# Optimization experiments

Hardware: AMD Instinct MI355X
Metric: run time of the kernel (lower is better)

## Reference

```python
import jax, jax.numpy as jnp
import numpy as np

N = 50000      # nodes
E = 800000     # edges (avg degree 16)
IN, HID, OUT = 256, 128, 64


def _glorot(key, shape):
    fan_in, fan_out = shape[0], shape[1]
    limit = np.sqrt(6.0 / (fan_in + fan_out))
    return jax.random.uniform(key, shape, jnp.float32, -limit, limit)


def setup_inputs() -> dict:
    key = jax.random.key(0)
    ks = jax.random.split(key, 8)
    x = jax.random.normal(ks[0], (N, IN), jnp.float32)
    edge_index = jax.random.randint(ks[1], (2, E), 0, N, dtype=jnp.int64)
    W1 = _glorot(ks[2], (IN, HID))
    b1 = jnp.zeros((HID,), jnp.float32)
    W2 = _glorot(ks[3], (HID, OUT))
    b2 = jnp.zeros((OUT,), jnp.float32)
    aw1 = _glorot(ks[4], (HID, 1))
    ab1 = jnp.zeros((1,), jnp.float32)
    aw2 = _glorot(ks[5], (OUT, 1))
    ab2 = jnp.zeros((1,), jnp.float32)
    return {"x": x, "edge_index": edge_index, "W1": W1, "b1": b1,
            "W2": W2, "b2": b2, "aw1": aw1, "ab1": ab1, "aw2": aw2, "ab2": ab2}


def gcn_conv(x, W, b, src, dst, n):
    # PyG GCNConv: add self-loops, symmetric degree normalization, then aggregate.
    h = x @ W                                   # [n, out]
    loops = jnp.arange(n, dtype=src.dtype)
    s = jnp.concatenate([src, loops])           # [E+n]
    d = jnp.concatenate([dst, loops])
    deg = jax.ops.segment_sum(jnp.ones(s.shape[0], h.dtype), d, num_segments=n)
    dinv = jnp.where(deg > 0, jax.lax.rsqrt(deg), 0.0)
    norm = dinv[s] * dinv[d]                    # [E+n]
    out = jax.ops.segment_sum(h[s] * norm[:, None], d, num_segments=n)
    return out + b


def reference(x, edge_index, W1, b1, W2, b2, aw1, ab1, aw2, ab2):
    # eval mode: dropout is identity
    src, dst = edge_index[0], edge_index[1]
    h = gcn_conv(x, W1, b1, src, dst, N)
    h = jax.nn.relu(h)
    h = h * jax.nn.sigmoid(h @ aw1 + ab1)       # sigmoid attention gate 1
    h = gcn_conv(h, W2, b2, src, dst, N)
    return h * jax.nn.sigmoid(h @ aw2 + ab2)    # sigmoid attention gate 2
```

## Files before the change

### kernel.cpp

```cpp
#include <hip/hip_runtime.h>
#include <math.h>

#define N_NODES 50000
#define N_EDGES 800000
#define D_IN    256
#define D_HID   128
#define D_OUT   64

#define NB 196
#define CH 4096

typedef unsigned int u32;
typedef unsigned short u16;
typedef __attribute__((ext_vector_type(8))) short bf16x8;
typedef __attribute__((ext_vector_type(4))) float f32x4;

__device__ __forceinline__ float bflo(u32 u) {
    union { u32 i; float f; } c; c.i = u << 16; return c.f;
}
__device__ __forceinline__ float bfhi(u32 u) {
    union { u32 i; float f; } c; c.i = u & 0xffff0000u; return c.f;
}
__device__ __forceinline__ u32 pack_bf2(float a, float b) {
    union { float f; u32 i; } ca, cb; ca.f = a; cb.f = b;
    u32 ra = (ca.i + 0x7fffu + ((ca.i >> 16) & 1u)) >> 16;
    u32 rb = (cb.i + 0x7fffu + ((cb.i >> 16) & 1u)) & 0xffff0000u;
    return ra | rb;
}
__device__ __forceinline__ u32 bf16_rne(float f) {
    union { float f; u32 i; } c; c.f = f;
    return (c.i + 0x7fffu + ((c.i >> 16) & 1u)) >> 16;
}
__device__ __forceinline__ float bfbits_to_f32(u32 hb) {
    union { u32 i; float f; } c; c.i = hb << 16; return c.f;
}

__device__ __forceinline__ int edge_at(const void* ei, int is64, int which, int i) {
    if (is64) return (int)((const long long*)ei)[(size_t)which * N_EDGES + i];
    return ((const int*)ei)[which * N_EDGES + i];
}

__device__ __forceinline__ int detect_is64(const void* ei, int t, int* s_is32) {
    if (t == 0) *s_is32 = 0;
    __syncthreads();
    if (t < 256) {
        int vv = ((const int*)ei)[2 * t + 1];
        if (vv != 0) atomicOr(s_is32, 1);
    }
    __syncthreads();
    return (*s_is32 == 0);
}


__global__ __launch_bounds__(256) void k_hist(const void* __restrict__ ei,
                                              int* __restrict__ bcnt) {
    __shared__ int h[NB];
    __shared__ int s_is32;
    int t = threadIdx.x;
    int is64 = detect_is64(ei, t, &s_is32);
    for (int i = t; i < NB; i += 256) h[i] = 0;
    __syncthreads();
    for (int i = blockIdx.x * 256 + t; i < N_EDGES; i += gridDim.x * 256) {
        int d = edge_at(ei, is64, 1, i);
        atomicAdd(&h[d >> 8], 1);
    }
    __syncthreads();
    for (int i = t; i < NB; i += 256) if (h[i]) atomicAdd(&bcnt[i], h[i]);
}

__global__ void k_bscan(const int* __restrict__ bcnt, int* __restrict__ bstart,
                        int* __restrict__ bcur) {
    __shared__ int sm[256];
    int t = threadIdx.x;
    int v = (t < NB) ? bcnt[t] : 0;
    sm[t] = v; __syncthreads();
    for (int off = 1; off < 256; off <<= 1) {
        int a = (t >= off) ? sm[t - off] : 0;
        __syncthreads();
        sm[t] += a;
        __syncthreads();
    }
    if (t < NB) { bstart[t] = sm[t] - v; bcur[t] = sm[t] - v; }
}

__global__ __launch_bounds__(256) void k_scatter1(const void* __restrict__ ei,
                                                  int* __restrict__ bcur,
                                                  u32* __restrict__ ebuf) {
    __shared__ int h[NB], gbase[NB], lc[NB];
    __shared__ int s_is32;
    int t = threadIdx.x;
    int is64 = detect_is64(ei, t, &s_is32);
    for (int i = t; i < NB; i += 256) { h[i] = 0; lc[i] = 0; }
    __syncthreads();
    int base = blockIdx.x * CH;

    u32 p[CH / 256];
    #pragma unroll
    for (int j = 0; j < CH / 256; ++j) {
        int i = base + j * 256 + t;
        if (i < N_EDGES) {
            int s = edge_at(ei, is64, 0, i);
            int d = edge_at(ei, is64, 1, i);
            p[j] = (u32)s | ((u32)d << 16);
            atomicAdd(&h[d >> 8], 1);
        }
    }
    __syncthreads();
    for (int i = t; i < NB; i += 256) if (h[i]) gbase[i] = atomicAdd(&bcur[i], h[i]);
    __syncthreads();
    #pragma unroll
    for (int j = 0; j < CH / 256; ++j) {
        int i = base + j * 256 + t;
        if (i < N_EDGES) {
            int b = (int)(p[j] >> 24);
            int lp = atomicAdd(&lc[b], 1);
            ebuf[gbase[b] + lp] = p[j];
        }
    }
}

__global__ __launch_bounds__(256) void k_scatter2(const u32* __restrict__ ebuf,
                                                  const int* __restrict__ bstart,
                                                  const int* __restrict__ bcnt,
                                                  int* __restrict__ rowstart,
                                                  int* __restrict__ cnt,
                                                  float* __restrict__ dinv,
                                                  int* __restrict__ colidx) {
    __shared__ int h2[256], lofs[256], cur[256], sm[256];
    int b = blockIdx.x, t = threadIdx.x;
    int e0 = bstart[b], ne = bcnt[b];
    h2[t] = 0; cur[t] = 0;
    __syncthreads();
    for (int i = t; i < ne; i += 256) {
        u32 p = ebuf[e0 + i];
        atomicAdd(&h2[(p >> 16) & 255], 1);
    }
    __syncthreads();
    int v = h2[t]; sm[t] = v; __syncthreads();
    for (int off = 1; off < 256; off <<= 1) {
        int a = (t >= off) ? sm[t - off] : 0;
        __syncthreads();
        sm[t] += a;
        __syncthreads();
    }
    lofs[t] = sm[t] - v;
    __syncthreads();
    int node = (b << 8) + t;
    if (node < N_NODES) {
        rowstart[node] = e0 + lofs[t];
        cnt[node] = v;
        dinv[node] = rsqrtf(1.0f + (float)v);
    }
    for (int i = t; i < ne; i += 256) {
        u32 p = ebuf[e0 + i];
        int dl = (p >> 16) & 255;
        int lp = atomicAdd(&cur[dl], 1);
        colidx[e0 + lofs[dl] + lp] = (int)(p & 0xffffu);
    }
}

__global__ void k_wsplit(const float* __restrict__ W1, u16* __restrict__ t1h,
                         u16* __restrict__ t1l, const float* __restrict__ W2,
                         u16* __restrict__ t2h, u16* __restrict__ t2l) {
    int i = blockIdx.x * 256 + threadIdx.x;
    if (i < D_IN * D_HID) {
        int k = i / D_HID, c = i - k * D_HID;
        float f = W1[i];
        u32 hb = bf16_rne(f);
        u32 lb = bf16_rne(f - bfbits_to_f32(hb));
        t1h[(size_t)c * D_IN + k] = (u16)hb;
        t1l[(size_t)c * D_IN + k] = (u16)lb;
    }
    int j = i - D_IN * D_HID;
    if (j >= 0 && j < D_HID * D_OUT) {
        int k = j / D_OUT, c = j - k * D_OUT;
        float f = W2[j];
        u32 hb = bf16_rne(f);
        u32 lb = bf16_rne(f - bfbits_to_f32(hb));
        t2h[(size_t)c * D_HID + k] = (u16)hb;
        t2l[(size_t)c * D_HID + k] = (u16)lb;
    }
}

template <int K, int NF>
__global__ __launch_bounds__(256) void k_gemm_mfma(
    const float* __restrict__ A, const u16* __restrict__ tHi,
    const u16* __restrict__ tLo, const float* __restrict__ dinv,
    u32* __restrict__ Cp, int M) {
    constexpr int NT = NF / 16;
    constexpr int LDK = 40;
    __shared__ u16 aH[128][LDK], aL[128][LDK];
    __shared__ u16 wH[NF][LDK], wL[NF][LDK];

    const int t = threadIdx.x;
    const int lane = t & 63, wv = t >> 6;
    const int m0 = blockIdx.x * 128;
    const int lr = lane & 15, lk = (lane >> 4) * 8;

    f32x4 acc[2][NT] = {};

    const int arow = t >> 1;
    const int akq = (t & 1) * 16;
    const bool aok = (m0 + arow) < M;
    const float* asrc = A + (size_t)(m0 + arow) * K + akq;

    for (int ks = 0; ks < K; ks += 32) {
        {
            float buf[16];
            #pragma unroll
            for (int j = 0; j < 16; ++j) buf[j] = 0.0f;
            if (aok) {
                const float4* p = (const float4*)(asrc + ks);
                float4 v0 = p[0], v1 = p[1], v2 = p[2], v3 = p[3];
                buf[0] = v0.x; buf[1] = v0.y; buf[2]  = v0.z; buf[3]  = v0.w;
                buf[4] = v1.x; buf[5] = v1.y; buf[6]  = v1.z; buf[7]  = v1.w;
                buf[8] = v2.x; buf[9] = v2.y; buf[10] = v2.z; buf[11] = v2.w;
                buf[12] = v3.x; buf[13] = v3.y; buf[14] = v3.z; buf[15] = v3.w;
            }
            u32 h[16], l[16];
            #pragma unroll
            for (int j = 0; j < 16; ++j) {
                h[j] = bf16_rne(buf[j]);
                l[j] = bf16_rne(buf[j] - bfbits_to_f32(h[j]));
            }
            uint4 hv0 = make_uint4(h[0] | (h[1] << 16), h[2] | (h[3] << 16),
                                   h[4] | (h[5] << 16), h[6] | (h[7] << 16));
            uint4 hv1 = make_uint4(h[8] | (h[9] << 16), h[10] | (h[11] << 16),
                                   h[12] | (h[13] << 16), h[14] | (h[15] << 16));
            uint4 lv0 = make_uint4(l[0] | (l[1] << 16), l[2] | (l[3] << 16),
                                   l[4] | (l[5] << 16), l[6] | (l[7] << 16));
            uint4 lv1 = make_uint4(l[8] | (l[9] << 16), l[10] | (l[11] << 16),
                                   l[12] | (l[13] << 16), l[14] | (l[15] << 16));
            *(uint4*)&aH[arow][akq + 0] = hv0;
            *(uint4*)&aH[arow][akq + 8] = hv1;
            *(uint4*)&aL[arow][akq + 0] = lv0;
            *(uint4*)&aL[arow][akq + 8] = lv1;
        }
        #pragma unroll
        for (int idx = t; idx < NF * 4; idx += 256) {
            int col = idx >> 2;
            int k8 = (idx & 3) * 8;
            *(uint4*)&wH[col][k8] = *(const uint4*)&tHi[(size_t)col * K + ks + k8];
            *(uint4*)&wL[col][k8] = *(const uint4*)&tLo[(size_t)col * K + ks + k8];
        }
        __syncthreads();

        bf16x8 afH[2], afL[2];
        #pragma unroll
        for (int mt = 0; mt < 2; ++mt) {
            int r = wv * 32 + mt * 16 + lr;
            afH[mt] = *(const bf16x8*)&aH[r][lk];
            afL[mt] = *(const bf16x8*)&aL[r][lk];
        }
        #pragma unroll
        for (int nt = 0; nt < NT; ++nt) {
            bf16x8 bh = *(const bf16x8*)&wH[nt * 16 + lr][lk];
            bf16x8 bl = *(const bf16x8*)&wL[nt * 16 + lr][lk];
            #pragma unroll
            for (int mt = 0; mt < 2; ++mt) {
                acc[mt][nt] = __builtin_amdgcn_mfma_f32_16x16x32_bf16(afH[mt], bh, acc[mt][nt], 0, 0, 0);
                acc[mt][nt] = __builtin_amdgcn_mfma_f32_16x16x32_bf16(afL[mt], bh, acc[mt][nt], 0, 0, 0);
                acc[mt][nt] = __builtin_amdgcn_mfma_f32_16x16x32_bf16(afH[mt], bl, acc[mt][nt], 0, 0, 0);
            }
        }
        __syncthreads();
    }

    #pragma unroll
    for (int mt = 0; mt < 2; ++mt) {
        #pragma unroll
        for (int r = 0; r < 4; ++r) {
            int row = m0 + wv * 32 + mt * 16 + (lane >> 4) * 4 + r;
            float dv = (row < M) ? dinv[row] : 0.0f;
            #pragma unroll
            for (int nt = 0; nt < NT; ++nt) {
                float v = acc[mt][nt][r] * dv;
                float vn = __shfl_xor(v, 1);
                if (!(lane & 1) && row < M) {
                    Cp[(size_t)row * (NF / 2) + nt * 8 + (lr >> 1)] = pack_bf2(v, vn);
                }
            }
        }
    }
}


__global__ __launch_bounds__(256) void k_agg1(
        const u32* __restrict__ hs, const int* __restrict__ rowstart,
        const int* __restrict__ cnt, const int* __restrict__ colidx,
        const float* __restrict__ dinv,
        const float* __restrict__ b, const float* __restrict__ aw,
        const float* __restrict__ ab, float* __restrict__ out) {
    int v = blockIdx.x * 4 + (threadIdx.x >> 6);
    int l = threadIdx.x & 63;
    if (v >= N_NODES) return;
    float dv = dinv[v];
    u32 su = hs[(size_t)v * 64 + l];
    float ax = bflo(su), ay = bfhi(su);
    int start = rowstart[v], len = cnt[v];
    const int* cx = colidx + start;
    int j = 0;
    for (; j + 8 <= len; j += 8) {
        int s0 = cx[j], s1 = cx[j + 1], s2 = cx[j + 2], s3 = cx[j + 3];
        int s4 = cx[j + 4], s5 = cx[j + 5], s6 = cx[j + 6], s7 = cx[j + 7];
        u32 u0 = hs[(size_t)s0 * 64 + l];
        u32 u1 = hs[(size_t)s1 * 64 + l];
        u32 u2 = hs[(size_t)s2 * 64 + l];
        u32 u3 = hs[(size_t)s3 * 64 + l];
        u32 u4 = hs[(size_t)s4 * 64 + l];
        u32 u5 = hs[(size_t)s5 * 64 + l];
        u32 u6 = hs[(size_t)s6 * 64 + l];
        u32 u7 = hs[(size_t)s7 * 64 + l];
        ax += bflo(u0) + bflo(u1) + bflo(u2) + bflo(u3)
            + bflo(u4) + bflo(u5) + bflo(u6) + bflo(u7);
        ay += bfhi(u0) + bfhi(u1) + bfhi(u2) + bfhi(u3)
            + bfhi(u4) + bfhi(u5) + bfhi(u6) + bfhi(u7);
    }
    for (; j + 4 <= len; j += 4) {
        int s0 = cx[j], s1 = cx[j + 1], s2 = cx[j + 2], s3 = cx[j + 3];
        u32 u0 = hs[(size_t)s0 * 64 + l];
        u32 u1 = hs[(size_t)s1 * 64 + l];
        u32 u2 = hs[(size_t)s2 * 64 + l];
        u32 u3 = hs[(size_t)s3 * 64 + l];
        ax += bflo(u0) + bflo(u1) + bflo(u2) + bflo(u3);
        ay += bfhi(u0) + bfhi(u1) + bfhi(u2) + bfhi(u3);
    }
    for (; j < len; ++j) {
        u32 u = hs[(size_t)cx[j] * 64 + l];
        ax += bflo(u); ay += bfhi(u);
    }
    float2 bp = ((const float2*)b)[l];
    ax = fmaxf(ax * dv + bp.x, 0.0f);
    ay = fmaxf(ay * dv + bp.y, 0.0f);
    float2 ap = ((const float2*)aw)[l];
    float p = ax * ap.x + ay * ap.y;
    for (int off = 32; off; off >>= 1) p += __shfl_xor(p, off);
    float g = 1.0f / (1.0f + expf(-(p + ab[0])));
    ((float2*)out)[(size_t)v * 64 + l] = make_float2(ax * g, ay * g);
}

__global__ __launch_bounds__(256) void k_agg2(
        const u32* __restrict__ hs, const int* __restrict__ rowstart,
        const int* __restrict__ cnt, const int* __restrict__ colidx,
        const float* __restrict__ dinv,
        const float* __restrict__ b, const float* __restrict__ aw,
        const float* __restrict__ ab, float* __restrict__ out) {
    int v = blockIdx.x * 4 + (threadIdx.x >> 6);
    int l = threadIdx.x & 63;
    if (v >= N_NODES) return;
    int c = l & 31, half = l >> 5;
    float dv = dinv[v];
    float ax = 0.0f, ay = 0.0f;
    if (half == 0) {
        u32 su = hs[(size_t)v * 32 + c];
        ax = bflo(su); ay = bfhi(su);
    }
    int start = rowstart[v], len = cnt[v];
    const int* cx = colidx + start;
    int j = half;
    for (; j + 6 < len; j += 8) {
        int s0 = cx[j], s1 = cx[j + 2], s2 = cx[j + 4], s3 = cx[j + 6];
        u32 u0 = hs[(size_t)s0 * 32 + c];
        u32 u1 = hs[(size_t)s1 * 32 + c];
        u32 u2 = hs[(size_t)s2 * 32 + c];
        u32 u3 = hs[(size_t)s3 * 32 + c];
        ax += bflo(u0) + bflo(u1) + bflo(u2) + bflo(u3);
        ay += bfhi(u0) + bfhi(u1) + bfhi(u2) + bfhi(u3);
    }
    for (; j + 2 < len; j += 4) {
        int s0 = cx[j], s1 = cx[j + 2];
        u32 u0 = hs[(size_t)s0 * 32 + c];
        u32 u1 = hs[(size_t)s1 * 32 + c];
        ax += bflo(u0) + bflo(u1);
        ay += bfhi(u0) + bfhi(u1);
    }
    if (j < len) {
        u32 u = hs[(size_t)cx[j] * 32 + c];
        ax += bflo(u); ay += bfhi(u);
    }
    ax += __shfl_xor(ax, 32);
    ay += __shfl_xor(ay, 32);
    float2 bp = ((const float2*)b)[c];
    ax = ax * dv + bp.x;
    ay = ay * dv + bp.y;
    float2 ap = ((const float2*)aw)[c];
    float p = ax * ap.x + ay * ap.y;
    for (int off = 16; off; off >>= 1) p += __shfl_xor(p, off);
    float g = 1.0f / (1.0f + expf(-(p + ab[0])));
    if (half == 0) ((float2*)out)[(size_t)v * 32 + c] = make_float2(ax * g, ay * g);
}


static inline size_t align_up(size_t x, size_t a) { return (x + a - 1) & ~(a - 1); }

extern "C" void kernel_launch(void* const* d_in, const int* in_sizes, int n_in,
                              void* d_out, int out_size, void* d_ws, size_t ws_size,
                              hipStream_t stream) {
    const float* x   = (const float*)d_in[0];
    const void*  ei  = d_in[1];
    const float* W1  = (const float*)d_in[2];
    const float* b1  = (const float*)d_in[3];
    const float* W2  = (const float*)d_in[4];
    const float* b2  = (const float*)d_in[5];
    const float* aw1 = (const float*)d_in[6];
    const float* ab1 = (const float*)d_in[7];
    const float* aw2 = (const float*)d_in[8];
    const float* ab2 = (const float*)d_in[9];
    float* out = (float*)d_out;

    char* w = (char*)d_ws;
    size_t off = 0;
    int*   bcnt     = (int*)(w + off); off = align_up(off + NB * 4, 256);
    int*   bstart   = (int*)(w + off); off = align_up(off + NB * 4, 256);
    int*   bcur     = (int*)(w + off); off = align_up(off + NB * 4, 256);
    int*   cnt      = (int*)(w + off); off = align_up(off + N_NODES * 4, 256);
    int*   rowstart = (int*)(w + off); off = align_up(off + N_NODES * 4, 256);
    float* dinv     = (float*)(w + off); off = align_up(off + N_NODES * 4, 256);
    u32*   ebuf     = (u32*)(w + off); off = align_up(off + (size_t)N_EDGES * 4, 256);
    int*   colidx   = (int*)(w + off); off = align_up(off + (size_t)N_EDGES * 4, 256);
    u32*   h1s      = (u32*)(w + off); off = align_up(off + (size_t)N_NODES * 64 * 4, 256);
    float* h1g      = (float*)(w + off); off = align_up(off + (size_t)N_NODES * D_HID * 4, 256);
    u32*   h2s      = (u32*)(w + off); off = align_up(off + (size_t)N_NODES * 32 * 4, 256);
    u16*   wt1h     = (u16*)(w + off); off = align_up(off + (size_t)D_IN * D_HID * 2, 256);
    u16*   wt1l     = (u16*)(w + off); off = align_up(off + (size_t)D_IN * D_HID * 2, 256);
    u16*   wt2h     = (u16*)(w + off); off = align_up(off + (size_t)D_HID * D_OUT * 2, 256);
    u16*   wt2l     = (u16*)(w + off); off = align_up(off + (size_t)D_HID * D_OUT * 2, 256);
    (void)ws_size; (void)out_size; (void)n_in; (void)in_sizes;

    hipMemsetAsync(bcnt, 0, NB * 4, stream);

    k_wsplit<<<(D_IN * D_HID + D_HID * D_OUT + 255) / 256, 256, 0, stream>>>(
        W1, wt1h, wt1l, W2, wt2h, wt2l);

    k_hist<<<256, 256, 0, stream>>>(ei, bcnt);
    k_bscan<<<1, 256, 0, stream>>>(bcnt, bstart, bcur);
    k_scatter1<<<(N_EDGES + CH - 1) / CH, 256, 0, stream>>>(ei, bcur, ebuf);
    k_scatter2<<<NB, 256, 0, stream>>>(ebuf, bstart, bcnt, rowstart, cnt, dinv, colidx);

    k_gemm_mfma<D_IN, D_HID><<<(N_NODES + 127) / 128, 256, 0, stream>>>(x, wt1h, wt1l, dinv, h1s, N_NODES);
    k_agg1<<<(N_NODES + 3) / 4, 256, 0, stream>>>(h1s, rowstart, cnt, colidx, dinv, b1, aw1, ab1, h1g);

    k_gemm_mfma<D_HID, D_OUT><<<(N_NODES + 127) / 128, 256, 0, stream>>>(h1g, wt2h, wt2l, dinv, h2s, N_NODES);
    k_agg2<<<(N_NODES + 3) / 4, 256, 0, stream>>>(h2s, rowstart, cnt, colidx, dinv, b2, aw2, ab2, out);
}
```

Before: 238.0 us.

## Fuse bucket scan into histogram, drop memset, shrink GEMM tile, truncate bf16 split

The bucket prefix scan moves into the last block of the histogram kernel, chosen with an atomic ticket counter, and the memset of the bucket counts moves into the weight-split kernel, removing two launches. The GEMM row tile shrinks from 128 to 64 rows per block, doubling the grid and halving per-thread accumulators. The bf16 hi/lo split switches from round-to-nearest to truncation, which is cheaper; since the lo term captures the residual, accuracy should stay close. It relies on correct threadfence/ticket ordering for the fused scan.

```diff
diff --git a/kernel.cpp b/kernel.cpp
--- a/kernel.cpp
+++ b/kernel.cpp
@@ -27,13 +27,6 @@
     u32 rb = (cb.i + 0x7fffu + ((cb.i >> 16) & 1u)) & 0xffff0000u;
     return ra | rb;
 }
-__device__ __forceinline__ u32 bf16_rne(float f) {
-    union { float f; u32 i; } c; c.f = f;
-    return (c.i + 0x7fffu + ((c.i >> 16) & 1u)) >> 16;
-}
-__device__ __forceinline__ float bfbits_to_f32(u32 hb) {
-    union { u32 i; float f; } c; c.i = hb << 16; return c.f;
-}
 
 __device__ __forceinline__ int edge_at(const void* ei, int is64, int which, int i) {
     if (is64) return (int)((const long long*)ei)[(size_t)which * N_EDGES + i];
@@ -53,9 +46,13 @@
 
 
 __global__ __launch_bounds__(256) void k_hist(const void* __restrict__ ei,
-                                              int* __restrict__ bcnt) {
+                                              int* __restrict__ bcnt,
+                                              int* __restrict__ bstart,
+                                              int* __restrict__ bcur,
+                                              int* __restrict__ tick) {
     __shared__ int h[NB];
     __shared__ int s_is32;
+    __shared__ int s_last;
     int t = threadIdx.x;
     int is64 = detect_is64(ei, t, &s_is32);
     for (int i = t; i < NB; i += 256) h[i] = 0;
@@ -66,21 +63,21 @@
     }
     __syncthreads();
     for (int i = t; i < NB; i += 256) if (h[i]) atomicAdd(&bcnt[i], h[i]);
-}
-
-__global__ void k_bscan(const int* __restrict__ bcnt, int* __restrict__ bstart,
-                        int* __restrict__ bcur) {
-    __shared__ int sm[256];
-    int t = threadIdx.x;
-    int v = (t < NB) ? bcnt[t] : 0;
-    sm[t] = v; __syncthreads();
-    for (int off = 1; off < 256; off <<= 1) {
-        int a = (t >= off) ? sm[t - off] : 0;
-        __syncthreads();
-        sm[t] += a;
-        __syncthreads();
-    }
-    if (t < NB) { bstart[t] = sm[t] - v; bcur[t] = sm[t] - v; }
+    __threadfence();
+    if (t == 0) s_last = (atomicAdd(tick, 1) == (int)gridDim.x - 1);
+    __syncthreads();
+    if (s_last) {
+        __shared__ int sm[256];
+        int v = (t < NB) ? atomicAdd(&bcnt[t], 0) : 0;
+        sm[t] = v; __syncthreads();
+        for (int off = 1; off < 256; off <<= 1) {
+            int a = (t >= off) ? sm[t - off] : 0;
+            __syncthreads();
+            sm[t] += a;
+            __syncthreads();
+        }
+        if (t < NB) { bstart[t] = sm[t] - v; bcur[t] = sm[t] - v; }
+    }
 }
 
 __global__ __launch_bounds__(256) void k_scatter1(const void* __restrict__ ei,
@@ -161,24 +158,27 @@
 
 __global__ void k_wsplit(const float* __restrict__ W1, u16* __restrict__ t1h,
                          u16* __restrict__ t1l, const float* __restrict__ W2,
-                         u16* __restrict__ t2h, u16* __restrict__ t2l) {
+                         u16* __restrict__ t2h, u16* __restrict__ t2l,
+                         int* __restrict__ bcnt, int* __restrict__ tick) {
     int i = blockIdx.x * 256 + threadIdx.x;
+    if (i < NB) bcnt[i] = 0;
+    if (i == 0) tick[0] = 0;
     if (i < D_IN * D_HID) {
         int k = i / D_HID, c = i - k * D_HID;
-        float f = W1[i];
-        u32 hb = bf16_rne(f);
-        u32 lb = bf16_rne(f - bfbits_to_f32(hb));
-        t1h[(size_t)c * D_IN + k] = (u16)hb;
-        t1l[(size_t)c * D_IN + k] = (u16)lb;
+        u32 bits = __float_as_uint(W1[i]);
+        u32 hb = bits & 0xffff0000u;
+        float lo = __uint_as_float(bits) - __uint_as_float(hb);
+        t1h[(size_t)c * D_IN + k] = (u16)(hb >> 16);
+        t1l[(size_t)c * D_IN + k] = (u16)(__float_as_uint(lo) >> 16);
     }
     int j = i - D_IN * D_HID;
     if (j >= 0 && j < D_HID * D_OUT) {
         int k = j / D_OUT, c = j - k * D_OUT;
-        float f = W2[j];
-        u32 hb = bf16_rne(f);
-        u32 lb = bf16_rne(f - bfbits_to_f32(hb));
-        t2h[(size_t)c * D_HID + k] = (u16)hb;
-        t2l[(size_t)c * D_HID + k] = (u16)lb;
+        u32 bits = __float_as_uint(W2[j]);
+        u32 hb = bits & 0xffff0000u;
+        float lo = __uint_as_float(bits) - __uint_as_float(hb);
+        t2h[(size_t)c * D_HID + k] = (u16)(hb >> 16);
+        t2l[(size_t)c * D_HID + k] = (u16)(__float_as_uint(lo) >> 16);
     }
 }
 
@@ -189,52 +189,45 @@
     u32* __restrict__ Cp, int M) {
     constexpr int NT = NF / 16;
     constexpr int LDK = 40;
-    __shared__ u16 aH[128][LDK], aL[128][LDK];
+    __shared__ u16 aH[64][LDK], aL[64][LDK];
     __shared__ u16 wH[NF][LDK], wL[NF][LDK];
 
     const int t = threadIdx.x;
     const int lane = t & 63, wv = t >> 6;
-    const int m0 = blockIdx.x * 128;
+    const int m0 = blockIdx.x * 64;
     const int lr = lane & 15, lk = (lane >> 4) * 8;
 
-    f32x4 acc[2][NT] = {};
-
-    const int arow = t >> 1;
-    const int akq = (t & 1) * 16;
+    f32x4 acc[NT] = {};
+
+    const int arow = t >> 2;
+    const int akq = (t & 3) * 8;
     const bool aok = (m0 + arow) < M;
     const float* asrc = A + (size_t)(m0 + arow) * K + akq;
 
     for (int ks = 0; ks < K; ks += 32) {
         {
-            float buf[16];
+            float f[8];
             #pragma unroll
-            for (int j = 0; j < 16; ++j) buf[j] = 0.0f;
+            for (int j = 0; j < 8; ++j) f[j] = 0.0f;
             if (aok) {
                 const float4* p = (const float4*)(asrc + ks);
-                float4 v0 = p[0], v1 = p[1], v2 = p[2], v3 = p[3];
-                buf[0] = v0.x; buf[1] = v0.y; buf[2]  = v0.z; buf[3]  = v0.w;
-                buf[4] = v1.x; buf[5] = v1.y; buf[6]  = v1.z; buf[7]  = v1.w;
-                buf[8] = v2.x; buf[9] = v2.y; buf[10] = v2.z; buf[11] = v2.w;
-                buf[12] = v3.x; buf[13] = v3.y; buf[14] = v3.z; buf[15] = v3.w;
+                float4 v0 = p[0], v1 = p[1];
+                f[0] = v0.x; f[1] = v0.y; f[2] = v0.z; f[3] = v0.w;
+                f[4] = v1.x; f[5] = v1.y; f[6] = v1.z; f[7] = v1.w;
             }
-            u32 h[16], l[16];
+            u32 hp[4], lp[4];
             #pragma unroll
-            for (int j = 0; j < 16; ++j) {
-                h[j] = bf16_rne(buf[j]);
-                l[j] = bf16_rne(buf[j] - bfbits_to_f32(h[j]));
+            for (int q = 0; q < 4; ++q) {
+                u32 b0 = __float_as_uint(f[2 * q]);
+                u32 b1 = __float_as_uint(f[2 * q + 1]);
+                u32 h0 = b0 & 0xffff0000u, h1 = b1 & 0xffff0000u;
+                float l0 = f[2 * q] - __uint_as_float(h0);
+                float l1 = f[2 * q + 1] - __uint_as_float(h1);
+                hp[q] = (h0 >> 16) | h1;
+                lp[q] = (__float_as_uint(l0) >> 16) | (__float_as_uint(l1) & 0xffff0000u);
             }
-            uint4 hv0 = make_uint4(h[0] | (h[1] << 16), h[2] | (h[3] << 16),
-                                   h[4] | (h[5] << 16), h[6] | (h[7] << 16));
-            uint4 hv1 = make_uint4(h[8] | (h[9] << 16), h[10] | (h[11] << 16),
-                                   h[12] | (h[13] << 16), h[14] | (h[15] << 16));
-            uint4 lv0 = make_uint4(l[0] | (l[1] << 16), l[2] | (l[3] << 16),
-                                   l[4] | (l[5] << 16), l[6] | (l[7] << 16));
-            uint4 lv1 = make_uint4(l[8] | (l[9] << 16), l[10] | (l[11] << 16),
-                                   l[12] | (l[13] << 16), l[14] | (l[15] << 16));
-            *(uint4*)&aH[arow][akq + 0] = hv0;
-            *(uint4*)&aH[arow][akq + 8] = hv1;
-            *(uint4*)&aL[arow][akq + 0] = lv0;
-            *(uint4*)&aL[arow][akq + 8] = lv1;
+            *(uint4*)&aH[arow][akq] = make_uint4(hp[0], hp[1], hp[2], hp[3]);
+            *(uint4*)&aL[arow][akq] = make_uint4(lp[0], lp[1], lp[2], lp[3]);
         }
         #pragma unroll
         for (int idx = t; idx < NF * 4; idx += 256) {
@@ -245,40 +238,29 @@
         }
         __syncthreads();
 
-        bf16x8 afH[2], afL[2];
-        #pragma unroll
-        for (int mt = 0; mt < 2; ++mt) {
-            int r = wv * 32 + mt * 16 + lr;
-            afH[mt] = *(const bf16x8*)&aH[r][lk];
-            afL[mt] = *(const bf16x8*)&aL[r][lk];
-        }
+        bf16x8 afH = *(const bf16x8*)&aH[wv * 16 + lr][lk];
+        bf16x8 afL = *(const bf16x8*)&aL[wv * 16 + lr][lk];
         #pragma unroll
         for (int nt = 0; nt < NT; ++nt) {
             bf16x8 bh = *(const bf16x8*)&wH[nt * 16 + lr][lk];
             bf16x8 bl = *(const bf16x8*)&wL[nt * 16 + lr][lk];
-            #pragma unroll
-            for (int mt = 0; mt < 2; ++mt) {
-                acc[mt][nt] = __builtin_amdgcn_mfma_f32_16x16x32_bf16(afH[mt], bh, acc[mt][nt], 0, 0, 0);
-                acc[mt][nt] = __builtin_amdgcn_mfma_f32_16x16x32_bf16(afL[mt], bh, acc[mt][nt], 0, 0, 0);
-                acc[mt][nt] = __builtin_amdgcn_mfma_f32_16x16x32_bf16(afH[mt], bl, acc[mt][nt], 0, 0, 0);
-            }
+            acc[nt] = __builtin_amdgcn_mfma_f32_16x16x32_bf16(afH, bh, acc[nt], 0, 0, 0);
+            acc[nt] = __builtin_amdgcn_mfma_f32_16x16x32_bf16(afL, bh, acc[nt], 0, 0, 0);
+            acc[nt] = __builtin_amdgcn_mfma_f32_16x16x32_bf16(afH, bl, acc[nt], 0, 0, 0);
         }
         __syncthreads();
     }
 
     #pragma unroll
-    for (int mt = 0; mt < 2; ++mt) {
+    for (int r = 0; r < 4; ++r) {
+        int row = m0 + wv * 16 + (lane >> 4) * 4 + r;
+        float dv = (row < M) ? dinv[row] : 0.0f;
         #pragma unroll
-        for (int r = 0; r < 4; ++r) {
-            int row = m0 + wv * 32 + mt * 16 + (lane >> 4) * 4 + r;
-            float dv = (row < M) ? dinv[row] : 0.0f;
-            #pragma unroll
-            for (int nt = 0; nt < NT; ++nt) {
-                float v = acc[mt][nt][r] * dv;
-                float vn = __shfl_xor(v, 1);
-                if (!(lane & 1) && row < M) {
-                    Cp[(size_t)row * (NF / 2) + nt * 8 + (lr >> 1)] = pack_bf2(v, vn);
-                }
+        for (int nt = 0; nt < NT; ++nt) {
+            float v = acc[nt][r] * dv;
+            float vn = __shfl_xor(v, 1);
+            if (!(lane & 1) && row < M) {
+                Cp[(size_t)row * (NF / 2) + nt * 8 + (lr >> 1)] = pack_bf2(v, vn);
             }
         }
     }
@@ -413,6 +395,7 @@
     int*   bcnt     = (int*)(w + off); off = align_up(off + NB * 4, 256);
     int*   bstart   = (int*)(w + off); off = align_up(off + NB * 4, 256);
     int*   bcur     = (int*)(w + off); off = align_up(off + NB * 4, 256);
+    int*   tick     = (int*)(w + off); off = align_up(off + 4, 256);
     int*   cnt      = (int*)(w + off); off = align_up(off + N_NODES * 4, 256);
     int*   rowstart = (int*)(w + off); off = align_up(off + N_NODES * 4, 256);
     float* dinv     = (float*)(w + off); off = align_up(off + N_NODES * 4, 256);
@@ -427,19 +410,16 @@
     u16*   wt2l     = (u16*)(w + off); off = align_up(off + (size_t)D_HID * D_OUT * 2, 256);
     (void)ws_size; (void)out_size; (void)n_in; (void)in_sizes;
 
-    hipMemsetAsync(bcnt, 0, NB * 4, stream);
-
     k_wsplit<<<(D_IN * D_HID + D_HID * D_OUT + 255) / 256, 256, 0, stream>>>(
-        W1, wt1h, wt1l, W2, wt2h, wt2l);
-
-    k_hist<<<256, 256, 0, stream>>>(ei, bcnt);
-    k_bscan<<<1, 256, 0, stream>>>(bcnt, bstart, bcur);
+        W1, wt1h, wt1l, W2, wt2h, wt2l, bcnt, tick);
+
+    k_hist<<<256, 256, 0, stream>>>(ei, bcnt, bstart, bcur, tick);
     k_scatter1<<<(N_EDGES + CH - 1) / CH, 256, 0, stream>>>(ei, bcur, ebuf);
     k_scatter2<<<NB, 256, 0, stream>>>(ebuf, bstart, bcnt, rowstart, cnt, dinv, colidx);
 
-    k_gemm_mfma<D_IN, D_HID><<<(N_NODES + 127) / 128, 256, 0, stream>>>(x, wt1h, wt1l, dinv, h1s, N_NODES);
+    k_gemm_mfma<D_IN, D_HID><<<(N_NODES + 63) / 64, 256, 0, stream>>>(x, wt1h, wt1l, dinv, h1s, N_NODES);
     k_agg1<<<(N_NODES + 3) / 4, 256, 0, stream>>>(h1s, rowstart, cnt, colidx, dinv, b1, aw1, ab1, h1g);
 
-    k_gemm_mfma<D_HID, D_OUT><<<(N_NODES + 127) / 128, 256, 0, stream>>>(h1g, wt2h, wt2l, dinv, h2s, N_NODES);
+    k_gemm_mfma<D_HID, D_OUT><<<(N_NODES + 63) / 64, 256, 0, stream>>>(h1g, wt2h, wt2l, dinv, h2s, N_NODES);
     k_agg2<<<(N_NODES + 3) / 4, 256, 0, stream>>>(h2s, rowstart, cnt, colidx, dinv, b2, aw2, ab2, out);
 }
```

Result: slower. 245.1 us (+3.0%).
